# Kernel tuning notes

Measured on AMD Instinct MI355X. Metric: run time of the kernel, lower is better.

## Reference

```python
import jax, jax.numpy as jnp
import numpy as np
from jax import lax

EPS = 1e-5
K = 3
PAD = 1
N_LAYERS = 7


def _conv2d(x, w, b):
    # x: [B,Cin,H,W], w: [Cout,Cin,K,K] -> [B,Cout,H,W], padding=1, stride=1
    y = lax.conv_general_dilated(x, w, window_strides=(1, 1),
                                 padding=[(PAD, PAD), (PAD, PAD)],
                                 dimension_numbers=('NCHW', 'OIHW', 'NCHW'))
    return y + b[None, :, None, None]


def _deform_conv2d(x, offset, weight):
    # torchvision deform_conv2d v1 (no mask, no bias), padding=PAD, stride=1.
    B, Cin, H, W = x.shape
    Cout = weight.shape[0]
    KK = K * K
    off = offset.reshape(B, KK, 2, H, W)
    dy = off[:, :, 0]  # [B,KK,H,W]
    dx = off[:, :, 1]
    kh = (jnp.arange(KK) // K).astype(x.dtype)  # row-major kernel taps
    kw = (jnp.arange(KK) % K).astype(x.dtype)
    hg = jnp.arange(H, dtype=x.dtype)
    wg = jnp.arange(W, dtype=x.dtype)
    # sampling positions p = p0 - pad + pk + offset
    py = dy + (hg[:, None] - PAD)[None, None, :, :] + kh[None, :, None, None]
    px = dx + (wg[None, :] - PAD)[None, None, :, :] + kw[None, :, None, None]
    y0 = jnp.floor(py)
    x0 = jnp.floor(px)
    ly = py - y0
    lx = px - x0
    y0i = y0.astype(jnp.int32)
    x0i = x0.astype(jnp.int32)

    def gather(img, yy, xx):  # img [Cin,H,W], yy/xx [KK,H,W]
        return img[:, yy, xx]  # [Cin,KK,H,W]

    gather_b = jax.vmap(gather)

    def corner(yi, xi, wgt):
        valid = (yi >= 0) & (yi < H) & (xi >= 0) & (xi < W)
        yc = jnp.clip(yi, 0, H - 1)
        xc = jnp.clip(xi, 0, W - 1)
        vals = gather_b(x, yc, xc)  # [B,Cin,KK,H,W]
        return vals * (wgt * valid)[:, None]

    sampled = (corner(y0i, x0i, (1 - ly) * (1 - lx))
               + corner(y0i, x0i + 1, (1 - ly) * lx)
               + corner(y0i + 1, x0i, ly * (1 - lx))
               + corner(y0i + 1, x0i + 1, ly * lx))  # [B,Cin,KK,H,W]
    return jnp.einsum('bikhw,oik->bohw', sampled, weight.reshape(Cout, Cin, KK))


def _layer(x, ow, ob, dw, g, b):
    offset = _conv2d(x, ow, ob)
    y = _deform_conv2d(x, offset, dw)
    # BatchNorm2d, training mode (batch stats, biased variance)
    mean = y.mean(axis=(0, 2, 3))
    var = y.var(axis=(0, 2, 3))
    yn = (y - mean[None, :, None, None]) * lax.rsqrt(var + EPS)[None, :, None, None]
    return jax.nn.relu(g[None, :, None, None] * yn + b[None, :, None, None])


def setup_inputs() -> dict:
    key = jax.random.key(0)
    ks = jax.random.split(key, 4)
    B, C, H, W = 4, 64, 128, 128
    x = jax.random.normal(ks[0], (B, C, H, W), dtype=jnp.float32)
    offset_w = jax.random.normal(ks[1], (N_LAYERS, 2 * K * K, C, K, K), dtype=jnp.float32) * 0.02
    offset_b = jnp.zeros((N_LAYERS, 2 * K * K), dtype=jnp.float32)
    deform_w = jax.random.normal(ks[2], (N_LAYERS, C, C, K, K), dtype=jnp.float32) * 0.05
    gamma = jnp.ones((N_LAYERS, C), dtype=jnp.float32)
    beta = jnp.zeros((N_LAYERS, C), dtype=jnp.float32)
    return {"x": x, "offset_w": offset_w, "offset_b": offset_b,
            "deform_w": deform_w, "gamma": gamma, "beta": beta}


def reference(x, offset_w, offset_b, deform_w, gamma, beta):
    def L(i, t):
        return _layer(t, offset_w[i], offset_b[i], deform_w[i], gamma[i], beta[i])
    # layer index map: 0=1_1, 1=1_2, 2=1_3, 3=1_4, 4=2_1, 5=2_2, 6=3
    out_1 = L(1, L(0, x))
    out_2 = L(4, x)
    out_sum_1 = out_1 + out_2
    out_1 = L(3, L(2, out_sum_1))
    out_2 = L(5, out_sum_1)
    out_3 = L(6, out_sum_1)
    return out_1 + out_2 + out_3
```

## Files before the change

### kernel.cpp

```cpp
#include <hip/hip_runtime.h>
#include <hip/hip_bf16.h>
#include <hip/hip_fp16.h>

#define NTOT 4194304
typedef __attribute__((ext_vector_type(4)))  short short4v;
typedef __attribute__((ext_vector_type(8)))  short short8v;
typedef __attribute__((ext_vector_type(4)))  float f32x4;
typedef __attribute__((ext_vector_type(2)))  float fx2;
typedef __attribute__((ext_vector_type(4)))  unsigned int uint4v;

__device__ __forceinline__ ushort f2bf(float f){
    __hip_bfloat16 h = __float2bfloat16(f);
    return __bfloat16_as_ushort(h);
}
__device__ __forceinline__ float bf2f(ushort u){
    return __uint_as_float(((unsigned)u)<<16);
}

__global__ __launch_bounds__(256) void pack_w(
    const float* __restrict__ dw, const float* __restrict__ ow,
    ushort* __restrict__ dwPk, ushort* __restrict__ owPk,
    float* __restrict__ statsG)
{
    int i = blockIdx.x*256 + threadIdx.x;
    if (i < 286720) {
        int j = i&3, co = (i>>2)&63, jg=(i>>8)&1, cih=(i>>9)&1, koff=(i>>10)&1;
        int r = i>>11; int kkp = r%5; int r2 = r/5; int ciq = r2&3; int l = r2>>2;
        int kk = kkp*2+koff, ci = ciq*16 + cih*8 + jg*4 + j;
        float v = (kk<9)? dw[((l*64+co)*64+ci)*9+kk] : 0.f;
        dwPk[i] = f2bf(v);
    }
    if (i < 143360) {
        int j = i&3, co = (i>>2)&31, jg=(i>>7)&1, cih=(i>>8)&1, koff=(i>>9)&1;
        int r = i>>10; int kkp = r%5; int r2 = r/5; int ciq = r2&3; int l = r2>>2;
        int kk = kkp*2+koff, ci = ciq*16 + cih*8 + jg*4 + j;
        float v = (kk<9 && co<18)? ow[((l*18+co)*64+ci)*9+kk] : 0.f;
        owPk[i] = f2bf(v);
    }
    if (i < 7*1024) statsG[i] = 0.f;
}

__global__ __launch_bounds__(256) void transpose_x(
    const float* __restrict__ src, ushort* __restrict__ xT)
{
    __shared__ ushort lds[128*72];
    const int bid = blockIdx.x, t = threadIdx.x;
    const int b = bid>>7, y = bid&127;
    const float* sp = src + (b<<20) + (y<<7);
#pragma unroll
    for (int i=0;i<32;i++){
        int lin = i*256 + t;
        int ci = lin>>7, xx = lin&127;
        lds[xx*72 + ci] = f2bf(sp[(ci<<14) + xx]);
    }
    __syncthreads();
    ushort* dp = xT + (((b<<7)+y)<<13);
#pragma unroll
    for (int i=0;i<4;i++){
        int u = i*256 + t;
        int xx = u>>3, cg = u&7;
        short8v v8 = *(const short8v*)(lds + xx*72 + cg*8);
        *(short8v*)(dp + (xx<<6) + cg*8) = v8;
    }
}

__constant__ int KHt[10] = {0,0,0,1,1,1,2,2,2,2};
__constant__ int KWt[10] = {0,1,2,0,1,2,0,1,2,2};

__global__ __attribute__((amdgpu_flat_work_group_size(512,512), amdgpu_waves_per_eu(4,8)))
void dcn_layer(
    const ushort* __restrict__ xTA, const ushort* __restrict__ xTB,
    const ushort* __restrict__ owPkB, const float* __restrict__ obB,
    const ushort* __restrict__ dwPkB, ushort* __restrict__ ybA,
    ushort* __restrict__ ybX, float* __restrict__ statsB, int l0, int l1)
{
    __shared__ __align__(16) char smem[79360];
    __half* offh = (__half*)(smem + 69120);

    const int t = threadIdx.x, lane = t&63, w = t>>6;
    const int l15 = lane&15, lg = lane>>4;
    const int cih = lg&1, koff = lane>>5;
    const int bid = blockIdx.x;
    const int lsel = bid >> 8;
    const int tb = bid & 255;
    const int L = lsel ? l1 : l0;
    const ushort* owPk = owPkB + L*20480;
    const float*  ob   = obB   + L*18;
    const ushort* dwPk = dwPkB + L*40960;
    ushort* yb         = lsel ? ybX : ybA;
    float*  statsL     = statsB + L*1024;

    const int xcd = tb&7, idx = tb>>3;
    const int b = xcd>>1, vh = xcd&1;
    const int ht = vh*8 + (idx>>2), wt = idx&3;
    const int w0 = wt*32, h0 = ht*8;
    const int row = h0 + w;
    const int RLO = h0-5, CLO = w0-8;
    const ushort* xb = (lsel ? xTB : xTA) + (b<<20);

    const short8v zz8 = (short8v){0,0,0,0,0,0,0,0};
    auto stage = [&](int P){
#pragma unroll 1
        for (int i=0;i<7;i++){
            int d = i*512 + t;
            if (d < 3456) {
                int slot = d&3, sp = d>>2;
                int rowt = sp/48, colt = sp - rowt*48;
                int gy = RLO+rowt, gx = CLO+colt;
                bool ok = ((unsigned)gy<128u) && ((unsigned)gx<128u);
                int gyc = min(max(gy,0),127), gxc = min(max(gx,0),127);
                short8v v = *(const short8v*)(xb + (((gyc<<7)+gxc)<<6) + (P*4+slot)*8);
                if (!ok) v = zz8;
                *(short8v*)(smem + sp*80 + ((slot^(sp&3))<<4)) = v;
            }
        }
    };

    f32x4 oacc[2][2];
#pragma unroll
    for (int p=0;p<2;p++)
#pragma unroll
        for (int q=0;q<2;q++) oacc[p][q] = (f32x4){0.f,0.f,0.f,0.f};

#pragma unroll 1
    for (int P=0; P<2; ++P) {
        if (P) __syncthreads();
        stage(P);
        __syncthreads();
#pragma unroll 1
        for (int kkp=0; kkp<5; ++kkp) {
            int kkA = 2*kkp;
            int kkB2 = (kkA+1>8)?8:(kkA+1);
            int kh = koff ? KHt[kkB2] : KHt[kkA];
            int kw = koff ? KWt[kkB2] : KWt[kkA];
            int PC[2], M4[2];
#pragma unroll
            for (int p=0;p<2;p++){
                int sp = (w + kh + 4)*48 + (p*16 + l15 + kw + 7);
                PC[p] = sp*80; M4[p] = (sp&3)<<4;
            }
#pragma unroll
            for (int cil=0; cil<2; ++cil) {
                int u4 = (((cil<<1)|cih)<<4);
                short8v afr[2];
#pragma unroll
                for (int p=0;p<2;p++)
                    afr[p] = *(const short8v*)(smem + PC[p] + (u4 ^ M4[p]));
                const ushort* wop = owPk + (P*2+cil)*5120 + kkp*1024 + koff*512 + cih*256;
#pragma unroll
                for (int q=0;q<2;q++){
                    short4v b0 = *(const short4v*)(wop +       (q*16+l15)*4);
                    short4v b1 = *(const short4v*)(wop + 128 + (q*16+l15)*4);
                    short8v bb = __builtin_shufflevector(b0,b1,0,1,2,3,4,5,6,7);
#pragma unroll
                    for (int p=0;p<2;p++)
                        oacc[p][q] = __builtin_amdgcn_mfma_f32_16x16x32_bf16(afr[p], bb, oacc[p][q], 0,0,0);
                }
            }
        }
    }

    {
        float biasq[2];
#pragma unroll
        for (int q=0;q<2;q++){ int o = q*16+l15; biasq[q] = (o<18)? ob[o] : 0.f; }
#pragma unroll
        for (int p=0;p<2;p++)
#pragma unroll
            for (int q=0;q<2;q++){
                int o = q*16+l15;
                if (o < 18) {
#pragma unroll
                    for (int r=0;r<4;r++){
                        int pix = w*32 + p*16 + lg*4 + r;
                        offh[pix*20 + o] = __float2half(oacc[p][q][r] + biasq[q]);
                    }
                }
            }
    }

    f32x4 acc[2][4];
#pragma unroll
    for (int p=0;p<2;p++)
#pragma unroll
        for (int q=0;q<4;q++) acc[p][q] = (f32x4){0.f,0.f,0.f,0.f};

#pragma unroll 1
    for (int P=0; P<2; ++P) {
        __syncthreads();
        stage(P);
        __syncthreads();
#pragma unroll 1
        for (int kkp=0; kkp<5; ++kkp) {
            int kkA = 2*kkp;
            int kkB2 = (kkA+1>8)?8:(kkA+1);
            int kh = koff ? KHt[kkB2] : KHt[kkA];
            int kw = koff ? KWt[kkB2] : KWt[kkA];
            int kkX = koff ? kkB2 : kkA;
            float F00[2],F01[2],F10[2],F11[2];
            int PC0[2],PC1[2],PC2[2],PC3[2], M40[2],M41[2],M42[2],M43[2];
            bool FB[2];
#pragma unroll
            for (int p=0;p<2;p++){
                int pix = w*32 + p*16 + l15;
                unsigned odp = *(const unsigned*)((const char*)offh + pix*40 + 4*kkX);
                float dy = __half2float(__ushort_as_half((ushort)(odp & 0xffffu)));
                float dx = __half2float(__ushort_as_half((ushort)(odp >> 16)));
                float py = (float)(row + kh - 1) + dy;
                float px = (float)(w0 + p*16 + l15 + kw - 1) + dx;
                float fy = floorf(py), fx = floorf(px);
                float ly = py - fy, lx = px - fx;
                int y0 = (int)fy, x0 = (int)fx;
                int r0 = y0 - RLO, c0 = x0 - CLO;
                int r1 = r0 + 1,  c1 = c0 + 1;
                bool ty0 = ((unsigned)r0<18u), ty1 = ((unsigned)r1<18u);
                bool tx0 = ((unsigned)c0<48u), tx1 = ((unsigned)c1<48u);
                float w00 = (1.f-ly)*(1.f-lx), w01 = (1.f-ly)*lx;
                float w10 = ly*(1.f-lx),       w11 = ly*lx;
                F00[p] = (ty0&&tx0)? w00 : 0.f;
                F01[p] = (ty0&&tx1)? w01 : 0.f;
                F10[p] = (ty1&&tx0)? w10 : 0.f;
                F11[p] = (ty1&&tx1)? w11 : 0.f;
                int rc0 = min(max(r0,0),17), rc1 = min(max(r1,0),17);
                int xc0 = min(max(c0,0),47), xc1 = min(max(c1,0),47);
                int s00 = rc0*48+xc0, s01 = rc0*48+xc1, s10 = rc1*48+xc0, s11 = rc1*48+xc1;
                PC0[p]=s00*80; M40[p]=(s00&3)<<4;
                PC1[p]=s01*80; M41[p]=(s01&3)<<4;
                PC2[p]=s10*80; M42[p]=(s10&3)<<4;
                PC3[p]=s11*80; M43[p]=(s11&3)<<4;
                bool allIn = ty0 && ty1 && tx0 && tx1;
                FB[p] = !allIn && (y0>=-1)&&(y0<=127)&&(x0>=-1)&&(x0<=127);
            }
#pragma unroll
            for (int cil=0; cil<2; ++cil) {
                int ciq = P*2 + cil;
                int u4 = (((cil<<1)|cih)<<4);
                short8v afr[2];
#pragma unroll
                for (int p=0;p<2;p++){
                    uint4v q00 = *(const uint4v*)(smem + PC0[p] + (u4^M40[p]));
                    uint4v q01 = *(const uint4v*)(smem + PC1[p] + (u4^M41[p]));
                    uint4v q10 = *(const uint4v*)(smem + PC2[p] + (u4^M42[p]));
                    uint4v q11 = *(const uint4v*)(smem + PC3[p] + (u4^M43[p]));
                    fx2 Fa = {F00[p],F00[p]}, Fb = {F01[p],F01[p]};
                    fx2 Fc = {F10[p],F10[p]}, Fd = {F11[p],F11[p]};
                    fx2 sv2[4];
#pragma unroll
                    for (int k=0;k<4;k++){
                        fx2 xa = {__uint_as_float(q00[k]<<16), __uint_as_float(q00[k]&0xffff0000u)};
                        fx2 xb2= {__uint_as_float(q01[k]<<16), __uint_as_float(q01[k]&0xffff0000u)};
                        fx2 xc = {__uint_as_float(q10[k]<<16), __uint_as_float(q10[k]&0xffff0000u)};
                        fx2 xd = {__uint_as_float(q11[k]<<16), __uint_as_float(q11[k]&0xffff0000u)};
                        sv2[k] = xa*Fa + xb2*Fb + xc*Fc + xd*Fd;
                    }
                    if (__builtin_expect(FB[p], 0)) {
                        int pix = w*32 + p*16 + l15;
                        unsigned odp = *(const unsigned*)((const char*)offh + pix*40 + 4*kkX);
                        float dy = __half2float(__ushort_as_half((ushort)(odp & 0xffffu)));
                        float dx = __half2float(__ushort_as_half((ushort)(odp >> 16)));
                        float py = (float)(row + kh - 1) + dy;
                        float px = (float)(w0 + p*16 + l15 + kw - 1) + dx;
                        float fy = floorf(py), fx = floorf(px);
                        float ly = py - fy, lx = px - fx;
                        int y0 = (int)fy, x0 = (int)fx;
                        int r0 = y0 - RLO, c0 = x0 - CLO;
                        bool ty0 = ((unsigned)r0<18u), ty1 = ((unsigned)(r0+1)<18u);
                        bool tx0 = ((unsigned)c0<48u), tx1 = ((unsigned)(c0+1)<48u);
                        bool vy0 = ((unsigned)y0<128u), vy1 = ((unsigned)(y0+1)<128u);
                        bool vx0 = ((unsigned)x0<128u), vx1 = ((unsigned)(x0+1)<128u);
                        float w00 = (1.f-ly)*(1.f-lx), w01 = (1.f-ly)*lx;
                        float w10 = ly*(1.f-lx),       w11 = ly*lx;
                        float rw00 = (vy0&&vx0&&!(ty0&&tx0))? w00 : 0.f;
                        float rw01 = (vy0&&vx1&&!(ty0&&tx1))? w01 : 0.f;
                        float rw10 = (vy1&&vx0&&!(ty1&&tx0))? w10 : 0.f;
                        float rw11 = (vy1&&vx1&&!(ty1&&tx1))? w11 : 0.f;
                        int y0c=min(max(y0,0),127), y1c=min(max(y0+1,0),127);
                        int x0c=min(max(x0,0),127), x1c=min(max(x0+1,0),127);
                        int cofs = (ciq*2 + cih)*8;
                        short8v a0 = *(const short8v*)(xb + ((((y0c<<7)+x0c)<<6) + cofs));
                        short8v a1 = *(const short8v*)(xb + ((((y0c<<7)+x1c)<<6) + cofs));
                        short8v a2 = *(const short8v*)(xb + ((((y1c<<7)+x0c)<<6) + cofs));
                        short8v a3 = *(const short8v*)(xb + ((((y1c<<7)+x1c)<<6) + cofs));
#pragma unroll
                        for (int j=0;j<8;j++){
                            float add = rw00*bf2f((ushort)a0[j]) + rw01*bf2f((ushort)a1[j])
                                      + rw10*bf2f((ushort)a2[j]) + rw11*bf2f((ushort)a3[j]);
                            if (j&1) sv2[j>>1].y += add; else sv2[j>>1].x += add;
                        }
                    }
#pragma unroll
                    for (int k=0;k<4;k++){
                        afr[p][2*k]   = (short)f2bf(sv2[k].x);
                        afr[p][2*k+1] = (short)f2bf(sv2[k].y);
                    }
                }
                const ushort* wp = dwPk + ciq*10240 + kkp*2048 + koff*1024 + cih*512;
#pragma unroll
                for (int q=0;q<4;q++){
                    short4v b0 = *(const short4v*)(wp +       (q*16+l15)*4);
                    short4v b1 = *(const short4v*)(wp + 256 + (q*16+l15)*4);
                    short8v bb = __builtin_shufflevector(b0,b1,0,1,2,3,4,5,6,7);
                    acc[0][q] = __builtin_amdgcn_mfma_f32_16x16x32_bf16(afr[0], bb, acc[0][q], 0,0,0);
                    acc[1][q] = __builtin_amdgcn_mfma_f32_16x16x32_bf16(afr[1], bb, acc[1][q], 0,0,0);
                }
            }
        }
    }

    float* yt  = (float*)smem;
    float* red = (float*)(smem + 33280);
#pragma unroll
    for (int half=0; half<2; ++half){
        __syncthreads();
#pragma unroll
        for (int p=0;p<2;p++)
#pragma unroll
            for (int qq=0;qq<2;qq++)
                *(f32x4*)(yt + (qq*16+l15)*260 + w*32 + p*16 + lg*4) = acc[p][half*2+qq];
        __syncthreads();
#pragma unroll
        for (int i=0;i<2;i++){
            int u = i*512 + t;
            int co = u>>5, px8 = (u&31)*8;
            short8v v8;
#pragma unroll
            for (int e=0;e<8;e++) v8[e] = (short)f2bf(yt[co*260 + px8 + e]);
            *(short8v*)(yb + ((((b<<6) + half*32 + co)<<14)
                        + ((h0 + (px8>>5))<<7) + w0 + (px8&31))) = v8;
        }
        {
            float s=0.f, s2=0.f;
            int co = t&31, seg = t>>5;
            const float* bp = yt + co*260 + seg*16;
#pragma unroll
            for (int qd=0;qd<16;qd++){ float v = bp[qd]; s += v; s2 += v*v; }
            red[seg*32+co] = s; red[512 + seg*32+co] = s2;
        }
        __syncthreads();
        if (t < 64){
            int vv = t>>5, cc = t&31;
            float a = 0.f;
#pragma unroll
            for (int g=0;g<16;g++) a += red[vv*512 + g*32 + cc];
            atomicAdd(statsL + (tb&7)*128 + vv*64 + half*32 + cc, a);
        }
    }
}

__global__ __launch_bounds__(256) void norm_fuse(
    const ushort* __restrict__ yv, const float* __restrict__ statsL,
    const float* __restrict__ gamma, const float* __restrict__ beta,
    const ushort* __restrict__ addB, float* __restrict__ dstF,
    ushort* __restrict__ dstB, ushort* __restrict__ xTout, int mode)
{
    __shared__ float scs[64], shs[64];
    __shared__ ushort lt[128*72];
    const int bid = blockIdx.x, t = threadIdx.x;
    const int b = bid>>7, y = bid&127;
    if (t < 64){
        float sum=0.f, ssq=0.f;
#pragma unroll
        for (int s=0;s<8;s++){ sum += statsL[s*128+t]; ssq += statsL[s*128+64+t]; }
        float mean = sum*(1.f/65536.f);
        float var  = ssq*(1.f/65536.f) - mean*mean;
        float inv  = rsqrtf(var + 1e-5f);
        float sc = gamma[t]*inv;
        scs[t] = sc; shs[t] = beta[t] - mean*sc;
    }
    __syncthreads();
#pragma unroll
    for (int i=0;i<4;i++){
        int g = i*256 + t;
        int ch = g>>4, xg = (g&15)*8;
        long base = (long)(((b<<6)+ch)<<14) + (y<<7) + xg;
        short8v v8 = *(const short8v*)(yv + base);
        float sc = scs[ch], sh = shs[ch];
        float r[8];
#pragma unroll
        for (int e=0;e<8;e++) r[e] = fmaxf(bf2f((ushort)v8[e])*sc+sh, 0.f);
        if (mode & 2) {
            short8v a8 = *(const short8v*)(addB + base);
#pragma unroll
            for (int e=0;e<8;e++) r[e] += bf2f((ushort)a8[e]);
        }
        if (mode & 4) {
            const float4* op = (const float4*)(dstF + base);
            float4 a0 = op[0], a1 = op[1];
            r[0]+=a0.x; r[1]+=a0.y; r[2]+=a0.z; r[3]+=a0.w;
            r[4]+=a1.x; r[5]+=a1.y; r[6]+=a1.z; r[7]+=a1.w;
        }
        if (mode & 5) {
            float4* dp = (float4*)(dstF + base);
            dp[0] = make_float4(r[0],r[1],r[2],r[3]);
            dp[1] = make_float4(r[4],r[5],r[6],r[7]);
        }
        if (mode & 16) {
            short8v o8;
#pragma unroll
            for (int e=0;e<8;e++) o8[e] = (short)f2bf(r[e]);
            *(short8v*)(dstB + base) = o8;
        }
        if (mode & 8) {
#pragma unroll
            for (int e=0;e<8;e++) lt[(xg+e)*72 + ch] = f2bf(r[e]);
        }
    }
    if (mode & 8) {
        __syncthreads();
        ushort* dp = xTout + (((b<<7)+y)<<13);
#pragma unroll
        for (int i=0;i<4;i++){
            int u = i*256 + t;
            int xx = u>>3, cg = u&7;
            short8v v8 = *(const short8v*)(lt + xx*72 + cg*8);
            *(short8v*)(dp + (xx<<6) + cg*8) = v8;
        }
    }
}

__global__ __launch_bounds__(256) void norm3(
    const ushort* __restrict__ ya, const ushort* __restrict__ ybp,
    const ushort* __restrict__ yc, const float* __restrict__ statsG,
    const float* __restrict__ gamma, const float* __restrict__ beta,
    int la, int lb, int lc, float* __restrict__ out)
{
    __shared__ float sc3[3][64], sh3[3][64];
    const int bid = blockIdx.x, t = threadIdx.x;
    const int b = bid>>7, y = bid&127;
    if (t < 192){
        int set = t>>6, ch = t&63;
        int l = (set==0)? la : ((set==1)? lb : lc);
        const float* st = statsG + l*1024;
        float sum=0.f, ssq=0.f;
#pragma unroll
        for (int s=0;s<8;s++){ sum += st[s*128+ch]; ssq += st[s*128+64+ch]; }
        float mean = sum*(1.f/65536.f);
        float var  = ssq*(1.f/65536.f) - mean*mean;
        float inv  = rsqrtf(var + 1e-5f);
        float sc = gamma[l*64+ch]*inv;
        sc3[set][ch] = sc; sh3[set][ch] = beta[l*64+ch] - mean*sc;
    }
    __syncthreads();
#pragma unroll
    for (int i=0;i<4;i++){
        int g = i*256 + t;
        int ch = g>>4, xg = (g&15)*8;
        long base = (long)(((b<<6)+ch)<<14) + (y<<7) + xg;
        short8v a8 = *(const short8v*)(ya  + base);
        short8v b8 = *(const short8v*)(ybp + base);
        short8v c8 = *(const short8v*)(yc  + base);
        float sa = sc3[0][ch], ha = sh3[0][ch];
        float sb = sc3[1][ch], hb = sh3[1][ch];
        float sc = sc3[2][ch], hc = sh3[2][ch];
        float r[8];
#pragma unroll
        for (int e=0;e<8;e++)
            r[e] = fmaxf(bf2f((ushort)a8[e])*sa+ha, 0.f)
                 + fmaxf(bf2f((ushort)b8[e])*sb+hb, 0.f)
                 + fmaxf(bf2f((ushort)c8[e])*sc+hc, 0.f);
        float4* dp = (float4*)(out + base);
        dp[0] = make_float4(r[0],r[1],r[2],r[3]);
        dp[1] = make_float4(r[4],r[5],r[6],r[7]);
    }
}

extern "C" void kernel_launch(void* const* d_in, const int* in_sizes, int n_in,
                              void* d_out, int out_size, void* d_ws, size_t ws_size,
                              hipStream_t stream)
{
    const float* x  = (const float*)d_in[0];
    const float* ow = (const float*)d_in[1];
    const float* ob = (const float*)d_in[2];
    const float* dw = (const float*)d_in[3];
    const float* g  = (const float*)d_in[4];
    const float* be = (const float*)d_in[5];
    float* out = (float*)d_out;

    ushort* yb0    = (ushort*)d_ws;
    ushort* yb1    = yb0 + NTOT;
    ushort* t4b    = yb1 + NTOT;
    ushort* xA     = t4b + NTOT;
    ushort* xB     = xA + NTOT;
    float*  statsG = (float*)(xB + NTOT);
    ushort* dwPk   = (ushort*)(statsG + 7*1024);
    ushort* owPk   = dwPk + 286720;

    pack_w<<<1120, 256, 0, stream>>>(dw, ow, dwPk, owPk, statsG);
    transpose_x<<<512, 256, 0, stream>>>(x, xA);

    auto nf = [&](int l, const ushort* ybp, int mode, const ushort* addB,
                  float* dstF, ushort* dstB, ushort* xout){
        norm_fuse<<<512, 256, 0, stream>>>(ybp, statsG + l*1024, g + l*64, be + l*64,
                                           addB, dstF, dstB, xout, mode);
    };

    dcn_layer<<<512, 512, 0, stream>>>(xA, xA, owPk, ob, dwPk, yb0, yb1, statsG, 4, 0);
    nf(4, yb0,       16, nullptr, nullptr, t4b,    nullptr);
    nf(0, yb1,        8, nullptr, nullptr, nullptr, xB);
    dcn_layer<<<256, 512, 0, stream>>>(xB, xB, owPk, ob, dwPk, yb0, yb0, statsG, 1, 1);
    nf(1, yb0,       10, t4b,    nullptr, nullptr, xA);
    dcn_layer<<<512, 512, 0, stream>>>(xA, xA, owPk, ob, dwPk, yb0, yb1, statsG, 2, 5);
    nf(2, yb0,        8, nullptr, nullptr, nullptr, xB);
    dcn_layer<<<512, 512, 0, stream>>>(xB, xA, owPk, ob, dwPk, yb0, t4b, statsG, 3, 6);
    norm3<<<512, 256, 0, stream>>>(yb0, yb1, t4b, statsG, g, be, 3, 5, 6, out);
}
```

Measured before the change: 270.4 us.

## Pad activation slabs with zero halo and stage tiles via direct global-to-LDS loads

Activation buffers are stored with a zero-filled halo (138x144 padded NHWC slabs), so the staging loop no longer needs bounds checks or clamping. Tile staging uses global_load_lds to copy 16-byte chunks straight into shared memory, with the LDS row pitch changed from 80 to 64 bytes and a new XOR swizzle. This shrinks LDS use and removes register round-trips, which may raise occupancy. In exchange it adds a zero-fill kernel over the padded buffers, uses more workspace, and ties correctness to the wave-contiguous LDS layout that global_load_lds imposes.

```diff
diff --git a/kernel.cpp b/kernel.cpp
--- a/kernel.cpp
+++ b/kernel.cpp
@@ -3,6 +3,7 @@
 #include <hip/hip_fp16.h>
 
 #define NTOT 4194304
+#define XSLAB 1271808
 typedef __attribute__((ext_vector_type(4)))  short short4v;
 typedef __attribute__((ext_vector_type(8)))  short short8v;
 typedef __attribute__((ext_vector_type(4)))  float f32x4;
@@ -15,6 +16,17 @@
 }
 __device__ __forceinline__ float bf2f(ushort u){
     return __uint_as_float(((unsigned)u)<<16);
+}
+__device__ __forceinline__ void gld_lds16(const ushort* g, char* l){
+    __builtin_amdgcn_global_load_lds(
+        (const __attribute__((address_space(1))) unsigned*)(g),
+        (__attribute__((address_space(3))) unsigned*)(l), 16, 0, 0);
+}
+
+__global__ __launch_bounds__(256) void zero_fill(ushort* a, ushort* c){
+    int i = blockIdx.x*256 + threadIdx.x;
+    const short8v z = (short8v){0,0,0,0,0,0,0,0};
+    if (i < 4*XSLAB/8) { *(short8v*)(a + i*8) = z; *(short8v*)(c + i*8) = z; }
 }
 
 __global__ __launch_bounds__(256) void pack_w(
@@ -54,7 +66,7 @@
         lds[xx*72 + ci] = f2bf(sp[(ci<<14) + xx]);
     }
     __syncthreads();
-    ushort* dp = xT + (((b<<7)+y)<<13);
+    ushort* dp = xT + (size_t)b*XSLAB + (((y+5)*144 + 8)<<6);
 #pragma unroll
     for (int i=0;i<4;i++){
         int u = i*256 + t;
@@ -74,8 +86,8 @@
     const ushort* __restrict__ dwPkB, ushort* __restrict__ ybA,
     ushort* __restrict__ ybX, float* __restrict__ statsB, int l0, int l1)
 {
-    __shared__ __align__(16) char smem[79360];
-    __half* offh = (__half*)(smem + 69120);
+    __shared__ __align__(16) char smem[65536];
+    __half* offh = (__half*)(smem + 55296);
 
     const int t = threadIdx.x, lane = t&63, w = t>>6;
     const int l15 = lane&15, lg = lane>>4;
@@ -96,22 +108,19 @@
     const int w0 = wt*32, h0 = ht*8;
     const int row = h0 + w;
     const int RLO = h0-5, CLO = w0-8;
-    const ushort* xb = (lsel ? xTB : xTA) + (b<<20);
-
-    const short8v zz8 = (short8v){0,0,0,0,0,0,0,0};
+    const ushort* xb = (lsel ? xTB : xTA) + (size_t)b*XSLAB;
+
     auto stage = [&](int P){
 #pragma unroll 1
         for (int i=0;i<7;i++){
             int d = i*512 + t;
             if (d < 3456) {
-                int slot = d&3, sp = d>>2;
+                int sp = d>>2, gph = d&3;
                 int rowt = sp/48, colt = sp - rowt*48;
                 int gy = RLO+rowt, gx = CLO+colt;
-                bool ok = ((unsigned)gy<128u) && ((unsigned)gx<128u);
-                int gyc = min(max(gy,0),127), gxc = min(max(gx,0),127);
-                short8v v = *(const short8v*)(xb + (((gyc<<7)+gxc)<<6) + (P*4+slot)*8);
-                if (!ok) v = zz8;
-                *(short8v*)(smem + sp*80 + ((slot^(sp&3))<<4)) = v;
+                int usrc = gph ^ ((sp>>1)&3);
+                const ushort* gp = xb + ((((gy+5)*144 + (gx+8))<<6) + (P*4+usrc)*8);
+                gld_lds16(gp, smem + ((i*512 + (t & ~63))<<4));
             }
         }
     };
@@ -137,7 +146,7 @@
 #pragma unroll
             for (int p=0;p<2;p++){
                 int sp = (w + kh + 4)*48 + (p*16 + l15 + kw + 7);
-                PC[p] = sp*80; M4[p] = (sp&3)<<4;
+                PC[p] = sp<<6; M4[p] = ((sp>>1)&3)<<4;
             }
 #pragma unroll
             for (int cil=0; cil<2; ++cil) {
@@ -224,10 +233,10 @@
                 int rc0 = min(max(r0,0),17), rc1 = min(max(r1,0),17);
                 int xc0 = min(max(c0,0),47), xc1 = min(max(c1,0),47);
                 int s00 = rc0*48+xc0, s01 = rc0*48+xc1, s10 = rc1*48+xc0, s11 = rc1*48+xc1;
-                PC0[p]=s00*80; M40[p]=(s00&3)<<4;
-                PC1[p]=s01*80; M41[p]=(s01&3)<<4;
-                PC2[p]=s10*80; M42[p]=(s10&3)<<4;
-                PC3[p]=s11*80; M43[p]=(s11&3)<<4;
+                PC0[p]=s00<<6; M40[p]=((s00>>1)&3)<<4;
+                PC1[p]=s01<<6; M41[p]=((s01>>1)&3)<<4;
+                PC2[p]=s10<<6; M42[p]=((s10>>1)&3)<<4;
+                PC3[p]=s11<<6; M43[p]=((s11>>1)&3)<<4;
                 bool allIn = ty0 && ty1 && tx0 && tx1;
                 FB[p] = !allIn && (y0>=-1)&&(y0<=127)&&(x0>=-1)&&(x0<=127);
             }
@@ -276,11 +285,11 @@
                         float rw11 = (vy1&&vx1&&!(ty1&&tx1))? w11 : 0.f;
                         int y0c=min(max(y0,0),127), y1c=min(max(y0+1,0),127);
                         int x0c=min(max(x0,0),127), x1c=min(max(x0+1,0),127);
-                        int cofs = (ciq*2 + cih)*8;
-                        short8v a0 = *(const short8v*)(xb + ((((y0c<<7)+x0c)<<6) + cofs));
-                        short8v a1 = *(const short8v*)(xb + ((((y0c<<7)+x1c)<<6) + cofs));
-                        short8v a2 = *(const short8v*)(xb + ((((y1c<<7)+x0c)<<6) + cofs));
-                        short8v a3 = *(const short8v*)(xb + ((((y1c<<7)+x1c)<<6) + cofs));
+                        int cofs = ciq*16 + cih*8;
+                        short8v a0 = *(const short8v*)(xb + ((((y0c+5)*144+(x0c+8))<<6) + cofs));
+                        short8v a1 = *(const short8v*)(xb + ((((y0c+5)*144+(x1c+8))<<6) + cofs));
+                        short8v a2 = *(const short8v*)(xb + ((((y1c+5)*144+(x0c+8))<<6) + cofs));
+                        short8v a3 = *(const short8v*)(xb + ((((y1c+5)*144+(x1c+8))<<6) + cofs));
 #pragma unroll
                         for (int j=0;j<8;j++){
                             float add = rw00*bf2f((ushort)a0[j]) + rw01*bf2f((ushort)a1[j])
@@ -407,7 +416,7 @@
     }
     if (mode & 8) {
         __syncthreads();
-        ushort* dp = xTout + (((b<<7)+y)<<13);
+        ushort* dp = xTout + (size_t)b*XSLAB + (((y+5)*144 + 8)<<6);
 #pragma unroll
         for (int i=0;i<4;i++){
             int u = i*256 + t;
@@ -480,11 +489,12 @@
     ushort* yb1    = yb0 + NTOT;
     ushort* t4b    = yb1 + NTOT;
     ushort* xA     = t4b + NTOT;
-    ushort* xB     = xA + NTOT;
-    float*  statsG = (float*)(xB + NTOT);
+    ushort* xB     = xA + 4*(size_t)XSLAB;
+    float*  statsG = (float*)(xB + 4*(size_t)XSLAB);
     ushort* dwPk   = (ushort*)(statsG + 7*1024);
     ushort* owPk   = dwPk + 286720;
 
+    zero_fill<<<2484, 256, 0, stream>>>(xA, xB);
     pack_w<<<1120, 256, 0, stream>>>(dw, ow, dwPk, owPk, statsG);
     transpose_x<<<512, 256, 0, stream>>>(x, xA);
 
```

New measurement: 267.2 us. About the same (-1.2%).
